# Performance work log

Measured on AMD Instinct MI355X. Metric: run time of the kernel, lower is better.

## Reference

```python
import jax, jax.numpy as jnp
import numpy as np
from jax import lax

N_NODES = 10000
N_EDGES = 160000
F_NODE = 128
C_GCN = 64
S_SEQ = 32
T_SEQ = 96
H_LSTM = 128


def setup_inputs() -> dict:
    key = jax.random.key(0)
    ks = jax.random.split(key, 20)
    inp = {
        "sequences": jax.random.normal(ks[0], (N_NODES, T_SEQ, S_SEQ), jnp.float32),
        "edge_index": jax.random.randint(ks[1], (2, N_EDGES), 0, N_NODES, jnp.int64),
        "edge_attr": jax.random.uniform(ks[2], (N_EDGES, 1), jnp.float32),
        "node_features": jax.random.normal(ks[3], (N_NODES, F_NODE), jnp.float32),
        "node_indices": jax.random.randint(ks[4], (N_NODES,), 0, N_NODES, jnp.int64),
    }
    s_g = 1.0 / np.sqrt(F_NODE)
    inp["gcn_w"] = jax.random.uniform(ks[5], (F_NODE, C_GCN), jnp.float32, -s_g, s_g)
    inp["gcn_b"] = jnp.zeros((C_GCN,), jnp.float32)
    in0 = S_SEQ + C_GCN
    s_l = 1.0 / np.sqrt(H_LSTM)
    inp["w_ih0"] = jax.random.uniform(ks[6], (4 * H_LSTM, in0), jnp.float32, -s_l, s_l)
    inp["w_hh0"] = jax.random.uniform(ks[7], (4 * H_LSTM, H_LSTM), jnp.float32, -s_l, s_l)
    inp["b_ih0"] = jax.random.uniform(ks[8], (4 * H_LSTM,), jnp.float32, -s_l, s_l)
    inp["b_hh0"] = jax.random.uniform(ks[9], (4 * H_LSTM,), jnp.float32, -s_l, s_l)
    inp["w_ih1"] = jax.random.uniform(ks[10], (4 * H_LSTM, H_LSTM), jnp.float32, -s_l, s_l)
    inp["w_hh1"] = jax.random.uniform(ks[11], (4 * H_LSTM, H_LSTM), jnp.float32, -s_l, s_l)
    inp["b_ih1"] = jax.random.uniform(ks[12], (4 * H_LSTM,), jnp.float32, -s_l, s_l)
    inp["b_hh1"] = jax.random.uniform(ks[13], (4 * H_LSTM,), jnp.float32, -s_l, s_l)
    s_f = 1.0 / np.sqrt(H_LSTM)
    inp["fc_w"] = jax.random.uniform(ks[14], (1, H_LSTM), jnp.float32, -s_f, s_f)
    inp["fc_b"] = jnp.zeros((1,), jnp.float32)
    return inp


def gcn_conv(x, edge_index, w, b):
    """PyG GCNConv: out = D^{-1/2} (A + I) D^{-1/2} X W + b."""
    n = x.shape[0]
    xw = x @ w  # [N, C]
    loop = jnp.arange(n, dtype=edge_index.dtype)
    row = jnp.concatenate([edge_index[0], loop])  # source j
    col = jnp.concatenate([edge_index[1], loop])  # target i
    deg = jax.ops.segment_sum(jnp.ones_like(col, dtype=xw.dtype), col, num_segments=n)
    dinv = jnp.where(deg > 0, lax.rsqrt(deg), 0.0)
    norm = dinv[row] * dinv[col]  # [E+N]
    msg = xw[row] * norm[:, None]  # gather + scale
    out = jax.ops.segment_sum(msg, col, num_segments=n)  # scatter-add
    return out + b


def lstm_layer(x, w_ih, w_hh, b_ih, b_hh):
    """batch_first LSTM layer; torch gate order i,f,g,o. x: [N,T,I] -> [N,T,H]."""
    n, t, _ = x.shape
    h_dim = w_hh.shape[1]
    xg = jnp.einsum("nti,gi->ntg", x, w_ih) + b_ih + b_hh  # [N,T,4H]

    def step(carry, xt):
        h, c = carry
        g = xt + h @ w_hh.T
        i, f, gg, o = jnp.split(g, 4, axis=-1)
        c = jax.nn.sigmoid(f) * c + jax.nn.sigmoid(i) * jnp.tanh(gg)
        h = jax.nn.sigmoid(o) * jnp.tanh(c)
        return (h, c), h

    h0 = jnp.zeros((n, h_dim), x.dtype)
    _, hs = lax.scan(step, (h0, h0), jnp.swapaxes(xg, 0, 1))
    return jnp.swapaxes(hs, 0, 1)


def reference(sequences, edge_index, edge_attr, node_features, node_indices,
              gcn_w, gcn_b, w_ih0, w_hh0, b_ih0, b_hh0,
              w_ih1, w_hh1, b_ih1, b_hh1, fc_w, fc_b):
    # GCN over the static graph (dropout = identity in eval mode)
    gcn_out = gcn_conv(node_features, edge_index, gcn_w, gcn_b)  # [N, C]
    t = sequences.shape[1]
    gcn_rep = jnp.broadcast_to(gcn_out[:, None, :], (gcn_out.shape[0], t, gcn_out.shape[1]))
    combined = jnp.concatenate([sequences, gcn_rep], axis=-1)  # [N, T, S+C]
    h = lstm_layer(combined, w_ih0, w_hh0, b_ih0, b_hh0)
    h = lstm_layer(h, w_ih1, w_hh1, b_ih1, b_hh1)
    last = h[:, -1, :]  # [N, H]
    return last @ fc_w.T + fc_b  # [N, 1]
```

## Files before the change

kernel.cpp:

```cpp
#include <hip/hip_runtime.h>
#include <hip/hip_bf16.h>

typedef _Float16 half8 __attribute__((ext_vector_type(8)));
typedef float floatx4 __attribute__((ext_vector_type(4)));
typedef float floatx2 __attribute__((ext_vector_type(2)));

#define N_NODES 10000
#define F_NODE  128
#define C_GCN   64
#define N_EDGES 160000
#define T_SEQ   96
#define S_SEQ   32
#define HID     128
#define M_BLK   40
#define MT      3
#define SEQ_STRIDE 104
#define H_STRIDE   136
#define WAVE_STREAM 61440

__device__ __forceinline__ float fast_rcp(float x) { return __builtin_amdgcn_rcpf(x); }
__device__ __forceinline__ float sigm_f(float x) {
    return fast_rcp(1.0f + __expf(-x));
}
__device__ __forceinline__ float tanh_f(float x) {
    return 2.0f * fast_rcp(1.0f + __expf(-2.0f * x)) - 1.0f;
}

__global__ void k_gcn_xw(const float* __restrict__ nf, const float* __restrict__ w,
                         float* __restrict__ xw) {
    int tid = blockIdx.x * 256 + threadIdx.x;
    int n = tid >> 6, c = tid & 63;
    if (n >= N_NODES) return;
    float s = 0.f;
    #pragma unroll 8
    for (int k = 0; k < F_NODE; ++k) s = fmaf(nf[n * F_NODE + k], w[k * C_GCN + c], s);
    xw[n * C_GCN + c] = s;
}

__global__ void k_deg_init(float* __restrict__ deg) {
    int i = blockIdx.x * 256 + threadIdx.x;
    if (i < N_NODES) deg[i] = 1.0f;
}

__global__ void k_deg_count(const int* __restrict__ ei, float* __restrict__ deg) {
    int e = blockIdx.x * 256 + threadIdx.x;
    if (e < N_EDGES) atomicAdd(&deg[ei[N_EDGES + e]], 1.0f);
}

__global__ void k_dinv(const float* __restrict__ deg, float* __restrict__ dinv) {
    int i = blockIdx.x * 256 + threadIdx.x;
    if (i < N_NODES) dinv[i] = rsqrtf(deg[i]);
}

__global__ void k_gcn_self(const float* __restrict__ xw, const float* __restrict__ dinv,
                           const float* __restrict__ gb, float* __restrict__ gout) {
    int tid = blockIdx.x * 256 + threadIdx.x;
    int n = tid >> 6, c = tid & 63;
    if (n >= N_NODES) return;
    float di = dinv[n];
    gout[tid] = xw[tid] * di * di + gb[c];
}

__global__ void k_gcn_scatter(const int* __restrict__ ei, const float* __restrict__ xw,
                              const float* __restrict__ dinv, float* __restrict__ gout) {
    int e = blockIdx.x * 4 + (threadIdx.x >> 6);
    int c = threadIdx.x & 63;
    if (e >= N_EDGES) return;
    int r  = ei[e];
    int cl = ei[N_EDGES + e];
    float nm = dinv[r] * dinv[cl];
    atomicAdd(&gout[cl * C_GCN + c], xw[r * C_GCN + c] * nm);
}

__global__ void k_pack(const float* __restrict__ w_ih0, const float* __restrict__ w_hh0,
                       const float* __restrict__ w_ih1, const float* __restrict__ w_hh1,
                       half8* __restrict__ pP) {
    int tid = blockIdx.x * 256 + threadIdx.x;
    if (tid >= 8 * 15 * 4 * 64) return;
    int lane = tid & 63;
    int g    = (tid >> 6) & 3;
    int s    = (tid >> 8) % 15;
    int w    = tid / 3840;
    const float* src; int kt, K;
    if (s < 3)       { src = w_ih0; kt = s;      K = 96;  }
    else if (s < 7)  { src = w_hh0; kt = s - 3;  K = 128; }
    else if (s < 11) { src = w_ih1; kt = s - 7;  K = 128; }
    else             { src = w_hh1; kt = s - 11; K = 128; }
    int row = g * 128 + w * 16 + (lane & 15);
    int k0  = kt * 32 + (lane >> 4) * 8;
    half8 v;
    #pragma unroll
    for (int j = 0; j < 8; ++j) v[j] = (_Float16)src[row * K + k0 + j];
    pP[tid] = v;
}

__global__ void k_bsum(const float* __restrict__ bi0, const float* __restrict__ bh0,
                       const float* __restrict__ bi1, const float* __restrict__ bh1,
                       float* __restrict__ bs) {
    int i = blockIdx.x * 256 + threadIdx.x;
    if (i < 512)       bs[i] = bi0[i] + bh0[i];
    else if (i < 1024) bs[i] = bi1[i - 512] + bh1[i - 512];
}

__device__ __forceinline__ void async_copy16(const void* g, void* l) {
    __builtin_amdgcn_global_load_lds(
        (const __attribute__((address_space(1))) unsigned int*)g,
        (__attribute__((address_space(3))) unsigned int*)l, 16, 0, 0);
}

__device__ __forceinline__ void dma_slot(const char* __restrict__ src, int lane, _Float16* slot) {
    #pragma unroll
    for (int g = 0; g < 4; ++g)
        async_copy16((const void*)(src + g * 1024 + lane * 16), (void*)(slot + g * 512));
}

__device__ __forceinline__ void mfma_kt(floatx4 acc[4][MT], const _Float16* slot, int lane,
                                        const _Float16* A, int strideA, int koff,
                                        int l15, int quad) {
    half8 bg[4], a[MT];
    #pragma unroll
    for (int g = 0; g < 4; ++g) bg[g] = *(const half8*)(slot + g * 512 + lane * 8);
    #pragma unroll
    for (int mt = 0; mt < MT; ++mt)
        a[mt] = *(const half8*)(A + (mt * 16 + l15) * strideA + koff + quad * 8);
    #pragma unroll
    for (int g = 0; g < 4; ++g)
        #pragma unroll
        for (int mt = 0; mt < MT; ++mt)
            acc[g][mt] = __builtin_amdgcn_mfma_f32_16x16x32_f16(a[mt], bg[g], acc[g][mt], 0, 0, 0);
}

__device__ __forceinline__ void epilogue(floatx4 acc[4][MT],
                                         float c[MT][4], _Float16* Hnext,
                                         int quad, int ch) {
    #pragma unroll
    for (int mt = 0; mt < MT; ++mt) {
        #pragma unroll
        for (int r = 0; r < 4; ++r) {
            float gi = acc[0][mt][r];
            float gf = acc[1][mt][r];
            float gg = acc[2][mt][r];
            float go = acc[3][mt][r];
            float cn = sigm_f(gf) * c[mt][r] + sigm_f(gi) * tanh_f(gg);
            c[mt][r] = cn;
            float h = sigm_f(go) * tanh_f(cn);
            Hnext[(mt * 16 + quad * 4 + r) * H_STRIDE + ch] = (_Float16)h;
        }
    }
}

__global__ __launch_bounds__(512, 2) void k_lstm(
    const float* __restrict__ seq, const float* __restrict__ gcn,
    const char* __restrict__ pW, const float* __restrict__ bsum,
    const float* __restrict__ fcw, const float* __restrict__ fcb,
    float* __restrict__ out) {

    __shared__ __align__(16) _Float16 sSeq[48 * SEQ_STRIDE];
    __shared__ __align__(16) _Float16 sH0[2][48 * H_STRIDE];
    __shared__ __align__(16) _Float16 sH1[2][48 * H_STRIDE];
    __shared__ __align__(16) _Float16 sW[2][8][2048];

    const int tid  = threadIdx.x;
    const int wid  = tid >> 6;
    const int lane = tid & 63;
    const int l15  = lane & 15;
    const int quad = lane >> 4;
    const int node0 = blockIdx.x * M_BLK;
    const int ch = wid * 16 + l15;

    const char* pWw = pW + wid * WAVE_STREAM;

    dma_slot(pWw, lane, &sW[0][wid][0]);

    for (int i = tid; i < 48 * SEQ_STRIDE; i += 512) sSeq[i] = (_Float16)0.f;
    for (int i = tid; i < 48 * H_STRIDE; i += 512) {
        sH0[0][i] = (_Float16)0.f; sH0[1][i] = (_Float16)0.f;
        sH1[0][i] = (_Float16)0.f; sH1[1][i] = (_Float16)0.f;
    }

    float bias0[4], bias1[4];
    #pragma unroll
    for (int g = 0; g < 4; ++g) {
        bias0[g] = bsum[g * 128 + ch];
        bias1[g] = bsum[512 + g * 128 + ch];
    }

    float c0[MT][4] = {{0}}, c1[MT][4] = {{0}};

    __syncthreads();

    for (int i = tid; i < M_BLK * (C_GCN / 2); i += 512) {
        int r = i >> 5, cp = (i & 31) * 2;
        floatx2 v = *(const floatx2*)(gcn + (size_t)(node0 + r) * C_GCN + cp);
        sSeq[r * SEQ_STRIDE + S_SEQ + cp]     = (_Float16)v.x;
        sSeq[r * SEQ_STRIDE + S_SEQ + cp + 1] = (_Float16)v.y;
    }
    {
        int r = tid >> 4, cp = (tid & 15) * 2;
        if (tid < M_BLK * 16) {
            floatx2 v = *(const floatx2*)(seq + ((size_t)(node0 + r) * T_SEQ) * S_SEQ + cp);
            sSeq[r * SEQ_STRIDE + cp]     = (_Float16)v.x;
            sSeq[r * SEQ_STRIDE + cp + 1] = (_Float16)v.y;
        }
    }
    __syncthreads();

    floatx4 acc[4][MT];
    const int pr = tid >> 4, pc = (tid & 15) * 2;
    int wb = 0;

    for (int t = 0; t < T_SEQ; ++t) {
        const int cur = t & 1, nxt = cur ^ 1;

        floatx2 pf0 = {0.f, 0.f}, pf1 = {0.f, 0.f};
        if (t + 1 < T_SEQ) {
            pf0 = *(const floatx2*)(seq + ((size_t)(node0 + pr) * T_SEQ + (t + 1)) * S_SEQ + pc);
            if (tid < 128) {
                int r1 = (512 + tid) >> 4, c1r = ((512 + tid) & 15) * 2;
                pf1 = *(const floatx2*)(seq + ((size_t)(node0 + r1) * T_SEQ + (t + 1)) * S_SEQ + c1r);
            }
        }

        #pragma unroll
        for (int g = 0; g < 4; ++g) {
            floatx4 bv = {bias0[g], bias0[g], bias0[g], bias0[g]};
            #pragma unroll
            for (int mt = 0; mt < MT; ++mt) acc[g][mt] = bv;
        }
        #pragma unroll
        for (int s = 0; s < 7; ++s) {
            dma_slot(pWw + (s + 1) * 4096, lane, &sW[wb ^ 1][wid][0]);
            if (s < 3)
                mfma_kt(acc, &sW[wb][wid][0], lane, sSeq, SEQ_STRIDE, s * 32, l15, quad);
            else
                mfma_kt(acc, &sW[wb][wid][0], lane, &sH0[cur][0], H_STRIDE, (s - 3) * 32, l15, quad);
            wb ^= 1;
        }
        epilogue(acc, c0, &sH0[nxt][0], quad, ch);
        __syncthreads();

        #pragma unroll
        for (int g = 0; g < 4; ++g) {
            floatx4 bv = {bias1[g], bias1[g], bias1[g], bias1[g]};
            #pragma unroll
            for (int mt = 0; mt < MT; ++mt) acc[g][mt] = bv;
        }
        #pragma unroll
        for (int s = 7; s < 15; ++s) {
            dma_slot(pWw + ((s + 1) % 15) * 4096, lane, &sW[wb ^ 1][wid][0]);
            if (s < 11)
                mfma_kt(acc, &sW[wb][wid][0], lane, &sH0[nxt][0], H_STRIDE, (s - 7) * 32, l15, quad);
            else
                mfma_kt(acc, &sW[wb][wid][0], lane, &sH1[cur][0], H_STRIDE, (s - 11) * 32, l15, quad);
            wb ^= 1;
        }
        if (t + 1 < T_SEQ) {
            sSeq[pr * SEQ_STRIDE + pc]     = (_Float16)pf0.x;
            sSeq[pr * SEQ_STRIDE + pc + 1] = (_Float16)pf0.y;
            if (tid < 128) {
                int r1 = (512 + tid) >> 4, c1r = ((512 + tid) & 15) * 2;
                sSeq[r1 * SEQ_STRIDE + c1r]     = (_Float16)pf1.x;
                sSeq[r1 * SEQ_STRIDE + c1r + 1] = (_Float16)pf1.y;
            }
        }
        epilogue(acc, c1, &sH1[nxt][0], quad, ch);
        __syncthreads();
    }

    if (tid < M_BLK) {
        const _Float16* h1 = &sH1[0][tid * H_STRIDE];
        float s = fcb[0];
        #pragma unroll 16
        for (int k = 0; k < HID; ++k) s = fmaf((float)h1[k], fcw[k], s);
        out[node0 + tid] = s;
    }
}

extern "C" void kernel_launch(void* const* d_in, const int* in_sizes, int n_in,
                              void* d_out, int out_size, void* d_ws, size_t ws_size,
                              hipStream_t stream) {
    const float* seq   = (const float*)d_in[0];
    const int*   ei    = (const int*)d_in[1];
    const float* nf    = (const float*)d_in[3];
    const float* gcn_w = (const float*)d_in[5];
    const float* gcn_b = (const float*)d_in[6];
    const float* w_ih0 = (const float*)d_in[7];
    const float* w_hh0 = (const float*)d_in[8];
    const float* b_ih0 = (const float*)d_in[9];
    const float* b_hh0 = (const float*)d_in[10];
    const float* w_ih1 = (const float*)d_in[11];
    const float* w_hh1 = (const float*)d_in[12];
    const float* b_ih1 = (const float*)d_in[13];
    const float* b_hh1 = (const float*)d_in[14];
    const float* fc_w  = (const float*)d_in[15];
    const float* fc_b  = (const float*)d_in[16];
    float* out = (float*)d_out;

    char* ws = (char*)d_ws;
    float* xw   = (float*)(ws);
    float* gout = (float*)(ws + 2621440);
    float* deg  = (float*)(ws + 5242880);
    float* dinv = (float*)(ws + 5283840);
    float* bsum = (float*)(ws + 5324800);
    char*  pP   = (char*)(ws + 5328896);

    k_gcn_xw     <<<2500,  256, 0, stream>>>(nf, gcn_w, xw);
    k_deg_init   <<<40,    256, 0, stream>>>(deg);
    k_deg_count  <<<625,   256, 0, stream>>>(ei, deg);
    k_dinv       <<<40,    256, 0, stream>>>(deg, dinv);
    k_gcn_self   <<<2500,  256, 0, stream>>>(xw, dinv, gcn_b, gout);
    k_gcn_scatter<<<40000, 256, 0, stream>>>(ei, xw, dinv, gout);

    k_pack<<<120, 256, 0, stream>>>(w_ih0, w_hh0, w_ih1, w_hh1, (half8*)pP);
    k_bsum<<<4,   256, 0, stream>>>(b_ih0, b_hh0, b_ih1, b_hh1, bsum);

    k_lstm<<<250, 512, 0, stream>>>(seq, gout, pP, bsum, fc_w, fc_b, out);
}
```

Baseline: 1.327 ms.

## Stream LSTM weight slots directly into registers with triple-buffered loads

Replaces the per-wave async global-to-LDS DMA of packed weight slots, plus the LDS reads that followed, with direct global loads into VGPRs. Three register buffers rotate so the next-but-one slot loads while the current one feeds MFMAs. This drops the sW LDS array and the LDS round trip, but raises register pressure (48 extra VGPRs of half8 data) under launch_bounds(512,2). It also exposes global-load latency to the MFMA chain, since only a one-slot lookahead hides it.

Result: slower. 1.792 ms (+35.1%).

```diff
diff --git a/kernel.cpp b/kernel.cpp
--- a/kernel.cpp
+++ b/kernel.cpp
@@ -102,33 +102,6 @@
     else if (i < 1024) bs[i] = bi1[i - 512] + bh1[i - 512];
 }
 
-__device__ __forceinline__ void async_copy16(const void* g, void* l) {
-    __builtin_amdgcn_global_load_lds(
-        (const __attribute__((address_space(1))) unsigned int*)g,
-        (__attribute__((address_space(3))) unsigned int*)l, 16, 0, 0);
-}
-
-__device__ __forceinline__ void dma_slot(const char* __restrict__ src, int lane, _Float16* slot) {
-    #pragma unroll
-    for (int g = 0; g < 4; ++g)
-        async_copy16((const void*)(src + g * 1024 + lane * 16), (void*)(slot + g * 512));
-}
-
-__device__ __forceinline__ void mfma_kt(floatx4 acc[4][MT], const _Float16* slot, int lane,
-                                        const _Float16* A, int strideA, int koff,
-                                        int l15, int quad) {
-    half8 bg[4], a[MT];
-    #pragma unroll
-    for (int g = 0; g < 4; ++g) bg[g] = *(const half8*)(slot + g * 512 + lane * 8);
-    #pragma unroll
-    for (int mt = 0; mt < MT; ++mt)
-        a[mt] = *(const half8*)(A + (mt * 16 + l15) * strideA + koff + quad * 8);
-    #pragma unroll
-    for (int g = 0; g < 4; ++g)
-        #pragma unroll
-        for (int mt = 0; mt < MT; ++mt)
-            acc[g][mt] = __builtin_amdgcn_mfma_f32_16x16x32_f16(a[mt], bg[g], acc[g][mt], 0, 0, 0);
-}
 
 __device__ __forceinline__ void epilogue(floatx4 acc[4][MT],
                                          float c[MT][4], _Float16* Hnext,
@@ -149,6 +122,25 @@
     }
 }
 
+#define LOAD_SLOT(B, S) do {                                        \
+    B[0] = *(const half8*)(pWw + (S) * 4096);                       \
+    B[1] = *(const half8*)(pWw + (S) * 4096 + 1024);                \
+    B[2] = *(const half8*)(pWw + (S) * 4096 + 2048);                \
+    B[3] = *(const half8*)(pWw + (S) * 4096 + 3072);                \
+} while (0)
+
+#define MFMA_KT(B, Aptr, strideA, koff) do {                        \
+    half8 _a[MT];                                                   \
+    _Pragma("unroll")                                               \
+    for (int _mt = 0; _mt < MT; ++_mt)                              \
+        _a[_mt] = *(const half8*)((Aptr) + (_mt * 16 + l15) * (strideA) + (koff) + quad * 8); \
+    _Pragma("unroll")                                               \
+    for (int _g = 0; _g < 4; ++_g)                                  \
+        _Pragma("unroll")                                           \
+        for (int _mt = 0; _mt < MT; ++_mt)                          \
+            acc[_g][_mt] = __builtin_amdgcn_mfma_f32_16x16x32_f16(_a[_mt], B[_g], acc[_g][_mt], 0, 0, 0); \
+} while (0)
+
 __global__ __launch_bounds__(512, 2) void k_lstm(
     const float* __restrict__ seq, const float* __restrict__ gcn,
     const char* __restrict__ pW, const float* __restrict__ bsum,
@@ -158,7 +150,6 @@
     __shared__ __align__(16) _Float16 sSeq[48 * SEQ_STRIDE];
     __shared__ __align__(16) _Float16 sH0[2][48 * H_STRIDE];
     __shared__ __align__(16) _Float16 sH1[2][48 * H_STRIDE];
-    __shared__ __align__(16) _Float16 sW[2][8][2048];
 
     const int tid  = threadIdx.x;
     const int wid  = tid >> 6;
@@ -168,9 +159,11 @@
     const int node0 = blockIdx.x * M_BLK;
     const int ch = wid * 16 + l15;
 
-    const char* pWw = pW + wid * WAVE_STREAM;
-
-    dma_slot(pWw, lane, &sW[0][wid][0]);
+    const char* pWw = pW + wid * WAVE_STREAM + lane * 16;
+
+    half8 b0[4], b1[4], b2[4];
+    LOAD_SLOT(b0, 0);
+    LOAD_SLOT(b1, 1);
 
     for (int i = tid; i < 48 * SEQ_STRIDE; i += 512) sSeq[i] = (_Float16)0.f;
     for (int i = tid; i < 48 * H_STRIDE; i += 512) {
@@ -206,19 +199,21 @@
     __syncthreads();
 
     floatx4 acc[4][MT];
-    const int pr = tid >> 4, pc = (tid & 15) * 2;
-    int wb = 0;
+    const int pr  = tid >> 4, pc = (tid & 15) * 2;
+    const int pr2 = (512 + tid) >> 4, pc2 = ((512 + tid) & 15) * 2;
 
     for (int t = 0; t < T_SEQ; ++t) {
         const int cur = t & 1, nxt = cur ^ 1;
+        const _Float16* h0c = &sH0[cur][0];
+        _Float16*       h0n = &sH0[nxt][0];
+        const _Float16* h1c = &sH1[cur][0];
+        _Float16*       h1n = &sH1[nxt][0];
 
         floatx2 pf0 = {0.f, 0.f}, pf1 = {0.f, 0.f};
         if (t + 1 < T_SEQ) {
             pf0 = *(const floatx2*)(seq + ((size_t)(node0 + pr) * T_SEQ + (t + 1)) * S_SEQ + pc);
-            if (tid < 128) {
-                int r1 = (512 + tid) >> 4, c1r = ((512 + tid) & 15) * 2;
-                pf1 = *(const floatx2*)(seq + ((size_t)(node0 + r1) * T_SEQ + (t + 1)) * S_SEQ + c1r);
-            }
+            if (tid < 128)
+                pf1 = *(const floatx2*)(seq + ((size_t)(node0 + pr2) * T_SEQ + (t + 1)) * S_SEQ + pc2);
         }
 
         #pragma unroll
@@ -227,16 +222,14 @@
             #pragma unroll
             for (int mt = 0; mt < MT; ++mt) acc[g][mt] = bv;
         }
-        #pragma unroll
-        for (int s = 0; s < 7; ++s) {
-            dma_slot(pWw + (s + 1) * 4096, lane, &sW[wb ^ 1][wid][0]);
-            if (s < 3)
-                mfma_kt(acc, &sW[wb][wid][0], lane, sSeq, SEQ_STRIDE, s * 32, l15, quad);
-            else
-                mfma_kt(acc, &sW[wb][wid][0], lane, &sH0[cur][0], H_STRIDE, (s - 3) * 32, l15, quad);
-            wb ^= 1;
-        }
-        epilogue(acc, c0, &sH0[nxt][0], quad, ch);
+        LOAD_SLOT(b2, 2);  MFMA_KT(b0, sSeq, SEQ_STRIDE, 0);
+        LOAD_SLOT(b0, 3);  MFMA_KT(b1, sSeq, SEQ_STRIDE, 32);
+        LOAD_SLOT(b1, 4);  MFMA_KT(b2, sSeq, SEQ_STRIDE, 64);
+        LOAD_SLOT(b2, 5);  MFMA_KT(b0, h0c, H_STRIDE, 0);
+        LOAD_SLOT(b0, 6);  MFMA_KT(b1, h0c, H_STRIDE, 32);
+        LOAD_SLOT(b1, 7);  MFMA_KT(b2, h0c, H_STRIDE, 64);
+        LOAD_SLOT(b2, 8);  MFMA_KT(b0, h0c, H_STRIDE, 96);
+        epilogue(acc, c0, h0n, quad, ch);
         __syncthreads();
 
         #pragma unroll
@@ -245,25 +238,24 @@
             #pragma unroll
             for (int mt = 0; mt < MT; ++mt) acc[g][mt] = bv;
         }
-        #pragma unroll
-        for (int s = 7; s < 15; ++s) {
-            dma_slot(pWw + ((s + 1) % 15) * 4096, lane, &sW[wb ^ 1][wid][0]);
-            if (s < 11)
-                mfma_kt(acc, &sW[wb][wid][0], lane, &sH0[nxt][0], H_STRIDE, (s - 7) * 32, l15, quad);
-            else
-                mfma_kt(acc, &sW[wb][wid][0], lane, &sH1[cur][0], H_STRIDE, (s - 11) * 32, l15, quad);
-            wb ^= 1;
-        }
+        LOAD_SLOT(b0, 9);   MFMA_KT(b1, h0n, H_STRIDE, 0);
+        LOAD_SLOT(b1, 10);  MFMA_KT(b2, h0n, H_STRIDE, 32);
+        LOAD_SLOT(b2, 11);  MFMA_KT(b0, h0n, H_STRIDE, 64);
+        LOAD_SLOT(b0, 12);  MFMA_KT(b1, h0n, H_STRIDE, 96);
+        LOAD_SLOT(b1, 13);  MFMA_KT(b2, h1c, H_STRIDE, 0);
+        LOAD_SLOT(b2, 14);  MFMA_KT(b0, h1c, H_STRIDE, 32);
+        LOAD_SLOT(b0, 0);   MFMA_KT(b1, h1c, H_STRIDE, 64);
+        LOAD_SLOT(b1, 1);   MFMA_KT(b2, h1c, H_STRIDE, 96);
+
         if (t + 1 < T_SEQ) {
             sSeq[pr * SEQ_STRIDE + pc]     = (_Float16)pf0.x;
             sSeq[pr * SEQ_STRIDE + pc + 1] = (_Float16)pf0.y;
             if (tid < 128) {
-                int r1 = (512 + tid) >> 4, c1r = ((512 + tid) & 15) * 2;
-                sSeq[r1 * SEQ_STRIDE + c1r]     = (_Float16)pf1.x;
-                sSeq[r1 * SEQ_STRIDE + c1r + 1] = (_Float16)pf1.y;
+                sSeq[pr2 * SEQ_STRIDE + pc2]     = (_Float16)pf1.x;
+                sSeq[pr2 * SEQ_STRIDE + pc2 + 1] = (_Float16)pf1.y;
             }
         }
-        epilogue(acc, c1, &sH1[nxt][0], quad, ch);
+        epilogue(acc, c1, h1n, quad, ch);
         __syncthreads();
     }
 
```

## Triple-buffer LSTM weight streaming with explicit vmcnt waits and lighter barriers

Applied to the files above, without the earlier changes.

Replaces the double-buffered per-wave weight slots with a three-slot ring, so two asynchronous global-to-LDS weight loads stay in flight while MFMAs consume the third slot. Explicit `s_waitcnt vmcnt(8)` waits replace the compiler's conservative full drains. `__syncthreads` becomes a barrier that waits only on LDS counters, so weight DMAs can cross the per-step barriers. The intent is to hide global or L2 weight-fetch latency in the recurrent loop. In exchange, LDS use grows to nearly the full per-CU budget, and correctness now relies on hand-counted vmcnt values.

Result: faster. 1.284 ms (-3.2%).

```diff
diff --git a/kernel.cpp b/kernel.cpp
--- a/kernel.cpp
+++ b/kernel.cpp
@@ -102,6 +102,7 @@
     else if (i < 1024) bs[i] = bi1[i - 512] + bh1[i - 512];
 }
 
+
 __device__ __forceinline__ void async_copy16(const void* g, void* l) {
     __builtin_amdgcn_global_load_lds(
         (const __attribute__((address_space(1))) unsigned int*)g,
@@ -113,6 +114,14 @@
     for (int g = 0; g < 4; ++g)
         async_copy16((const void*)(src + g * 1024 + lane * 16), (void*)(slot + g * 512));
 }
+
+#define VMWAIT8() asm volatile("s_waitcnt vmcnt(8)" ::: "memory")
+
+#define BARRIER_NOVM() do {                                   \
+    asm volatile("s_waitcnt lgkmcnt(0)" ::: "memory");        \
+    __builtin_amdgcn_s_barrier();                             \
+    asm volatile("" ::: "memory");                            \
+} while (0)
 
 __device__ __forceinline__ void mfma_kt(floatx4 acc[4][MT], const _Float16* slot, int lane,
                                         const _Float16* A, int strideA, int koff,
@@ -158,7 +167,9 @@
     __shared__ __align__(16) _Float16 sSeq[48 * SEQ_STRIDE];
     __shared__ __align__(16) _Float16 sH0[2][48 * H_STRIDE];
     __shared__ __align__(16) _Float16 sH1[2][48 * H_STRIDE];
-    __shared__ __align__(16) _Float16 sW[2][8][2048];
+    __shared__ __align__(16) _Float16 sWa[8][2048];
+    __shared__ __align__(16) _Float16 sWb[8][2048];
+    __shared__ __align__(16) _Float16 sWc[8][2048];
 
     const int tid  = threadIdx.x;
     const int wid  = tid >> 6;
@@ -170,7 +181,11 @@
 
     const char* pWw = pW + wid * WAVE_STREAM;
 
-    dma_slot(pWw, lane, &sW[0][wid][0]);
+#define DMA(S, RING)                  dma_slot(pWw + (S) * 4096, lane, &RING[wid][0])
+#define USE(RING, Aptr, stride, koff) mfma_kt(acc, &RING[wid][0], lane, (Aptr), (stride), (koff), l15, quad)
+
+    DMA(0, sWa);
+    DMA(1, sWb);
 
     for (int i = tid; i < 48 * SEQ_STRIDE; i += 512) sSeq[i] = (_Float16)0.f;
     for (int i = tid; i < 48 * H_STRIDE; i += 512) {
@@ -207,10 +222,13 @@
 
     floatx4 acc[4][MT];
     const int pr = tid >> 4, pc = (tid & 15) * 2;
-    int wb = 0;
 
     for (int t = 0; t < T_SEQ; ++t) {
         const int cur = t & 1, nxt = cur ^ 1;
+        const _Float16* h0c = &sH0[cur][0];
+        _Float16*       h0n = &sH0[nxt][0];
+        const _Float16* h1c = &sH1[cur][0];
+        _Float16*       h1n = &sH1[nxt][0];
 
         floatx2 pf0 = {0.f, 0.f}, pf1 = {0.f, 0.f};
         if (t + 1 < T_SEQ) {
@@ -227,17 +245,15 @@
             #pragma unroll
             for (int mt = 0; mt < MT; ++mt) acc[g][mt] = bv;
         }
-        #pragma unroll
-        for (int s = 0; s < 7; ++s) {
-            dma_slot(pWw + (s + 1) * 4096, lane, &sW[wb ^ 1][wid][0]);
-            if (s < 3)
-                mfma_kt(acc, &sW[wb][wid][0], lane, sSeq, SEQ_STRIDE, s * 32, l15, quad);
-            else
-                mfma_kt(acc, &sW[wb][wid][0], lane, &sH0[cur][0], H_STRIDE, (s - 3) * 32, l15, quad);
-            wb ^= 1;
-        }
-        epilogue(acc, c0, &sH0[nxt][0], quad, ch);
-        __syncthreads();
+        DMA(2, sWc);  VMWAIT8();  USE(sWa, sSeq, SEQ_STRIDE, 0);
+        DMA(3, sWa);  VMWAIT8();  USE(sWb, sSeq, SEQ_STRIDE, 32);
+        DMA(4, sWb);  VMWAIT8();  USE(sWc, sSeq, SEQ_STRIDE, 64);
+        DMA(5, sWc);  VMWAIT8();  USE(sWa, h0c, H_STRIDE, 0);
+        DMA(6, sWa);  VMWAIT8();  USE(sWb, h0c, H_STRIDE, 32);
+        DMA(7, sWb);  VMWAIT8();  USE(sWc, h0c, H_STRIDE, 64);
+        DMA(8, sWc);  VMWAIT8();  USE(sWa, h0c, H_STRIDE, 96);
+        epilogue(acc, c0, h0n, quad, ch);
+        BARRIER_NOVM();
 
         #pragma unroll
         for (int g = 0; g < 4; ++g) {
@@ -245,15 +261,15 @@
             #pragma unroll
             for (int mt = 0; mt < MT; ++mt) acc[g][mt] = bv;
         }
-        #pragma unroll
-        for (int s = 7; s < 15; ++s) {
-            dma_slot(pWw + ((s + 1) % 15) * 4096, lane, &sW[wb ^ 1][wid][0]);
-            if (s < 11)
-                mfma_kt(acc, &sW[wb][wid][0], lane, &sH0[nxt][0], H_STRIDE, (s - 7) * 32, l15, quad);
-            else
-                mfma_kt(acc, &sW[wb][wid][0], lane, &sH1[cur][0], H_STRIDE, (s - 11) * 32, l15, quad);
-            wb ^= 1;
-        }
+        DMA(9,  sWa); VMWAIT8();  USE(sWb, h0n, H_STRIDE, 0);
+        DMA(10, sWb); VMWAIT8();  USE(sWc, h0n, H_STRIDE, 32);
+        DMA(11, sWc); VMWAIT8();  USE(sWa, h0n, H_STRIDE, 64);
+        DMA(12, sWa); VMWAIT8();  USE(sWb, h0n, H_STRIDE, 96);
+        DMA(13, sWb); VMWAIT8();  USE(sWc, h1c, H_STRIDE, 0);
+        DMA(14, sWc); VMWAIT8();  USE(sWa, h1c, H_STRIDE, 32);
+        DMA(0,  sWa); VMWAIT8();  USE(sWb, h1c, H_STRIDE, 64);
+        DMA(1,  sWb); VMWAIT8();  USE(sWc, h1c, H_STRIDE, 96);
+
         if (t + 1 < T_SEQ) {
             sSeq[pr * SEQ_STRIDE + pc]     = (_Float16)pf0.x;
             sSeq[pr * SEQ_STRIDE + pc + 1] = (_Float16)pf0.y;
@@ -263,9 +279,14 @@
                 sSeq[r1 * SEQ_STRIDE + c1r + 1] = (_Float16)pf1.y;
             }
         }
-        epilogue(acc, c1, &sH1[nxt][0], quad, ch);
-        __syncthreads();
-    }
+        epilogue(acc, c1, h1n, quad, ch);
+        BARRIER_NOVM();
+    }
+
+#undef DMA
+#undef USE
+
+    asm volatile("s_waitcnt vmcnt(0)" ::: "memory");
 
     if (tid < M_BLK) {
         const _Float16* h1 = &sH1[0][tid * H_STRIDE];
```
